# Kernel tuning notes

Hardware: AMD Instinct MI355X
Metric: run time of the kernel (lower is better)

The kernel has to match this reference:

```python
import jax, jax.numpy as jnp
import numpy as np


def setup_inputs() -> dict:
    key = jax.random.key(0)
    k1, k2, k3 = jax.random.split(key, 3)
    B, C, H, W = 32, 768, 24, 24
    feat1 = jax.random.normal(k1, (B, C, H, W), dtype=jnp.float32)
    feat2 = jax.random.normal(k2, (B, C, H, W), dtype=jnp.float32)
    gamma = jax.random.normal(k3, (1,), dtype=jnp.float32)
    return {"feat1": feat1, "feat2": feat2, "gamma": gamma}


def reference(feat1, feat2, gamma):
    # CMA: channel-wise cross-modal attention over flattened spatial dim.
    B, C, H, W = feat1.shape
    q = feat1.reshape(B, C, H * W)          # [B, C, HW]
    kv = feat2.reshape(B, C, H * W)         # [B, C, HW] (k and v share this)
    attn = jnp.einsum('bcn,bdn->bcd', q, kv)          # [B, C, C] = q @ k^T
    attn = jax.nn.softmax(attn, axis=-1)
    info = jnp.einsum('bcd,bdn->bcn', attn, kv)       # [B, C, HW]
    info = info.reshape(B, C, H, W)
    return gamma[0] * info + feat1
```

## Files before the change

kernel.cpp:

```cpp
#include <hip/hip_runtime.h>

#define B_  32
#define C_  768
#define HW_ 576

#define NCQ 18
#define NCP 24

typedef _Float16 half8 __attribute__((ext_vector_type(8)));
typedef _Float16 half4 __attribute__((ext_vector_type(4)));
typedef float    f32x4 __attribute__((ext_vector_type(4)));

__device__ __forceinline__ void g2l16(const void* g, void* l) {
    __builtin_amdgcn_global_load_lds(
        (const __attribute__((address_space(1))) unsigned int*)g,
        (__attribute__((address_space(3))) unsigned int*)l, 16, 0, 0);
}

#define VM(N) asm volatile("s_waitcnt vmcnt(" #N ")" ::: "memory")

__global__ __launch_bounds__(256) void prep_all(const float* __restrict__ f1,
                                                const float* __restrict__ f2,
                                                char* __restrict__ q16,
                                                char* __restrict__ kv16,
                                                char* __restrict__ vt,
                                                int b0, int cur, int nqk) {
    __shared__ float Vsh[32 * 201];
    const int bid = blockIdx.x;
    if (bid < nqk) {
        const int bz = bid % cur, u = bid / cur;
        int g   = u * 256 + threadIdx.x;
        int x   = g & 3;
        int row = (g >> 2) & 127;
        int t3  = g >> 9;
        int k0  = t3 % 18;
        int ti  = t3 / 18;
        int kc  = x ^ ((row >> 1) & 3);
        size_t src = ((size_t)(b0 + bz) * C_ + ti * 128 + row) * HW_ + k0 * 32 + kc * 8;
        f32x4 a0 = *(const f32x4*)(f1 + src);
        f32x4 a1 = *(const f32x4*)(f1 + src + 4);
        f32x4 c0 = *(const f32x4*)(f2 + src);
        f32x4 c1 = *(const f32x4*)(f2 + src + 4);
        half8 ha, hb;
        #pragma unroll
        for (int e = 0; e < 4; ++e) {
            ha[e] = (_Float16)a0[e]; ha[4 + e] = (_Float16)a1[e];
            hb[e] = (_Float16)c0[e]; hb[4 + e] = (_Float16)c1[e];
        }
        size_t dst = ((size_t)(((size_t)bz * 6 + ti) * 18 + k0) << 9) | (g & 511);
        *(half8*)(q16  + dst * 16) = ha;
        *(half8*)(kv16 + dst * 16) = hb;
    } else {
        int bid2 = bid - nqk;
        const int bz = bid2 % cur, u = bid2 / cur;
        int k0 = u / 3, tj = u % 3;
        int b  = b0 + bz;
        int t  = threadIdx.x;
        #pragma unroll
        for (int p = 0; p < 6; ++p) {
            int fidx = p * 256 + t;
            int dd = fidx / 48, c4 = fidx % 48;
            f32x4 v = *(const f32x4*)(f2 + ((size_t)b * C_ + k0 * 32 + dd) * HW_ + tj * 192 + c4 * 4);
            #pragma unroll
            for (int e = 0; e < 4; ++e) Vsh[dd * 201 + c4 * 4 + e] = v[e];
        }
        __syncthreads();
        char* ob = vt + ((size_t)(bz * 3 + tj) * NCP + k0) * 12288;
        #pragma unroll
        for (int p = 0; p < 3; ++p) {
            int o = p * 256 + t;
            int x = o & 3, n = o >> 2;
            int kc = x ^ ((n >> 1) & 3);
            half8 h;
            #pragma unroll
            for (int j = 0; j < 8; ++j) h[j] = (_Float16)Vsh[(kc * 8 + j) * 201 + n];
            *(half8*)(ob + o * 16) = h;
        }
    }
}

__global__ __launch_bounds__(512, 4) void qk6(const char* __restrict__ q16,
                                              const char* __restrict__ kv16,
                                              float* __restrict__ attn,
                                              float2* __restrict__ part,
                                              int cur) {
    __shared__ __align__(16) char S[3][24576];
    const int wg = blockIdx.x;
    const int bz = wg % cur, u = wg / cur;
    const int ti = u >> 2, tj = u & 3;
    const int t = threadIdx.x, lane = t & 63, w = t >> 6;
    const int rsub = lane >> 2, cb = (lane & 3) * 16;

    const char *p0, *p1, *p2;
    int o0, o1, o2;
    {
        auto arow = [&](int l) {
            int gr = ti * 192 + 16 * l + rsub;
            return q16 + ((size_t)(bz * 6 + (gr >> 7)) * NCQ) * 8192 + (gr & 127) * 64 + cb;
        };
        auto brow = [&](int l) {
            int gd = tj * 192 + 16 * l + rsub;
            return kv16 + ((size_t)(bz * 6 + (gd >> 7)) * NCQ) * 8192 + (gd & 127) * 64 + cb;
        };
        if (w < 4) {
            p0 = arow(2 * w);     o0 = (2 * w) * 1024;
            p1 = arow(2 * w + 1); o1 = (2 * w + 1) * 1024;
            p2 = brow(8 + w);     o2 = 12288 + (8 + w) * 1024;
        } else {
            int v = w - 4;
            p0 = brow(2 * v);     o0 = 12288 + (2 * v) * 1024;
            p1 = brow(2 * v + 1); o1 = 12288 + (2 * v + 1) * 1024;
            p2 = arow(8 + v);     o2 = (8 + v) * 1024;
        }
    }

    const int wr = (w >> 1) * 48, wc = (w & 1) * 96;
    const int r16 = lane & 15, cg = lane >> 4;
    int offA[3], offB[6];
    #pragma unroll
    for (int m = 0; m < 3; ++m) {
        int ra = wr + m * 16 + r16;
        offA[m] = ra * 64 + ((cg ^ ((ra >> 1) & 3)) << 4);
    }
    #pragma unroll
    for (int n = 0; n < 6; ++n) {
        int rb = wc + n * 16 + r16;
        offB[n] = 12288 + rb * 64 + ((cg ^ ((rb >> 1) & 3)) << 4);
    }

    f32x4 acc[3][6] = {};

#define STG(SLOT) do {                          \
        char* sb_ = &S[SLOT][0];                \
        g2l16(p0, sb_ + o0);                    \
        g2l16(p1, sb_ + o1);                    \
        g2l16(p2, sb_ + o2);                    \
        p0 += 8192; p1 += 8192; p2 += 8192;     \
    } while (0)

    STG(0); STG(1);
    int rd = 0, st = 2;
    for (int c = 0; c < NCQ; ++c) {
        if (c + 2 < NCQ) {
            STG(st); st = (st == 2) ? 0 : st + 1;
            VM(6);
        } else if (c + 2 == NCQ) {
            VM(3);
        } else {
            VM(0);
        }
        __builtin_amdgcn_s_barrier();
        const char* sb = &S[rd][0];
        rd = (rd == 2) ? 0 : rd + 1;
        half8 a0 = *(const half8*)(sb + offA[0]);
        half8 a1 = *(const half8*)(sb + offA[1]);
        half8 a2 = *(const half8*)(sb + offA[2]);
        __builtin_amdgcn_s_setprio(1);
        #pragma unroll
        for (int n = 0; n < 6; ++n) {
            half8 bn = *(const half8*)(sb + offB[n]);
            acc[0][n] = __builtin_amdgcn_mfma_f32_16x16x32_f16(a0, bn, acc[0][n], 0, 0, 0);
            acc[1][n] = __builtin_amdgcn_mfma_f32_16x16x32_f16(a1, bn, acc[1][n], 0, 0, 0);
            acc[2][n] = __builtin_amdgcn_mfma_f32_16x16x32_f16(a2, bn, acc[2][n], 0, 0, 0);
        }
        __builtin_amdgcn_s_setprio(0);
        __builtin_amdgcn_s_barrier();
    }
#undef STG

    float* ab = attn + ((size_t)bz * C_ + ti * 192) * C_ + tj * 192;
    const int col = lane & 15, rbase = (lane >> 4) * 4;
    #pragma unroll
    for (int m = 0; m < 3; ++m)
        #pragma unroll
        for (int n = 0; n < 6; ++n)
            #pragma unroll
            for (int rg = 0; rg < 4; ++rg)
                ab[(size_t)(wr + m * 16 + rbase + rg) * C_ + wc + n * 16 + col] = acc[m][n][rg];

    const int half = w & 1;
    #pragma unroll
    for (int m = 0; m < 3; ++m)
        #pragma unroll
        for (int rg = 0; rg < 4; ++rg) {
            float mx = -1e30f;
            #pragma unroll
            for (int n = 0; n < 6; ++n) mx = fmaxf(mx, acc[m][n][rg]);
            #pragma unroll
            for (int o = 1; o < 16; o <<= 1) mx = fmaxf(mx, __shfl_xor(mx, o));
            float s = 0.f;
            #pragma unroll
            for (int n = 0; n < 6; ++n) s += __expf(acc[m][n][rg] - mx);
            #pragma unroll
            for (int o = 1; o < 16; o <<= 1) s += __shfl_xor(s, o);
            if ((lane & 15) == 0) {
                int row = wr + m * 16 + (lane >> 4) * 4 + rg;
                part[((size_t)bz * C_ + ti * 192 + row) * 8 + tj * 2 + half] =
                    make_float2(mx, s);
            }
        }
}

__global__ __launch_bounds__(256) void sm_combine(const float2* __restrict__ part,
                                                  float2* __restrict__ stats,
                                                  const float* __restrict__ gamma,
                                                  int cur) {
    const int bid = blockIdx.x;
    const int bz = bid % cur, u = bid / cur;
    const int R = bz * C_ + u * 256 + threadIdx.x;
    float2 p[8];
    #pragma unroll
    for (int i = 0; i < 8; ++i) p[i] = part[(size_t)R * 8 + i];
    float m = p[0].x;
    #pragma unroll
    for (int i = 1; i < 8; ++i) m = fmaxf(m, p[i].x);
    float s = 0.f;
    #pragma unroll
    for (int i = 0; i < 8; ++i) s += p[i].y * __expf(p[i].x - m);
    stats[R] = make_float2(m, gamma[0] / s);
}

__global__ __launch_bounds__(512, 4) void pv10(const float* __restrict__ attn,
                                               const char* __restrict__ vt,
                                               const float2* __restrict__ stats,
                                               const float* __restrict__ f1,
                                               float* __restrict__ out,
                                               int b0, int cur) {
    __shared__ __align__(16) char S[4][20480];
    const int wg = blockIdx.x;
    const int bz = wg % cur, u = wg / cur;
    const int ti = u / 3, tj = u % 3;
    const int t = threadIdx.x, lane = t & 63, w = t >> 6;
    const int rsub = lane >> 2, cbb = (lane & 3) * 16;

    const int r0 = t >> 3;
    const int r1 = 64 + r0;
    const int d4 = t & 7;
    const float* srcA0 = attn + ((size_t)bz * C_ + ti * 128 + r0) * C_ + d4 * 4;
    const float* srcA1 = attn + ((size_t)bz * C_ + ti * 128 + r1) * C_ + d4 * 4;
    const float2 ms0 = stats[bz * C_ + ti * 128 + r0];
    const float2 ms1 = stats[bz * C_ + ti * 128 + r1];
    const int aw0 = r0 * 64 + (((d4 >> 1) ^ ((r0 >> 1) & 3)) << 4) + (d4 & 1) * 8;
    const int aw1 = r1 * 64 + (((d4 >> 1) ^ ((r1 >> 1) & 3)) << 4) + (d4 & 1) * 8;

    const char* vbase = vt + ((size_t)(bz * 3 + tj) * NCP) * 12288;
    const char *pB0, *pB1;
    int ob0, ob1;
    if (w < 4) {
        pB0 = vbase + (32 * w + rsub) * 64 + cbb;          ob0 = 8192 + (32 * w) * 64;
        pB1 = vbase + (32 * w + 16 + rsub) * 64 + cbb;     ob1 = 8192 + (32 * w + 16) * 64;
    } else {
        pB0 = vbase + (128 + 16 * (w - 4) + rsub) * 64 + cbb;
        ob0 = 8192 + (128 + 16 * (w - 4)) * 64;
        pB1 = vbase; ob1 = 0;
    }

    const int wr = (w >> 2) * 64, wc = (w & 3) * 48;
    const int r16 = lane & 15, cg = lane >> 4;
    int offA[4], offB[3];
    #pragma unroll
    for (int m = 0; m < 4; ++m) {
        int ra = wr + m * 16 + r16;
        offA[m] = ra * 64 + ((cg ^ ((ra >> 1) & 3)) << 4);
    }
    #pragma unroll
    for (int n = 0; n < 3; ++n) {
        int rb = wc + n * 16 + r16;
        offB[n] = 8192 + rb * 64 + ((cg ^ ((rb >> 1) & 3)) << 4);
    }

    f32x4 acc[4][3] = {};
    f32x4 vaA0, vaA1;
    f32x4 vaB0, vaB1;

#define STG_B(SLOT) do {                                  \
        g2l16(pB0, &S[SLOT][0] + ob0); pB0 += 12288;      \
        if (w < 4) { g2l16(pB1, &S[SLOT][0] + ob1); pB1 += 12288; } \
    } while (0)
#define LD_A(V0, V1) do { V0 = *(const f32x4*)srcA0; V1 = *(const f32x4*)srcA1; \
                          srcA0 += 32; srcA1 += 32; } while (0)
#define WR_A(SLOT, V0, V1) do {                                        \
        half4 h0, h1;                                                  \
        _Pragma("unroll")                                              \
        for (int e = 0; e < 4; ++e) {                                  \
            h0[e] = (_Float16)(__expf(V0[e] - ms0.x) * ms0.y);         \
            h1[e] = (_Float16)(__expf(V1[e] - ms1.x) * ms1.y);         \
        }                                                              \
        *(half4*)(&S[SLOT][0] + aw0) = h0;                             \
        *(half4*)(&S[SLOT][0] + aw1) = h1;                             \
    } while (0)
#define MFMA_SLOT(SB) do {                                             \
        const char* sb_ = (SB);                                        \
        half8 a_[4], b_[3];                                            \
        _Pragma("unroll")                                              \
        for (int m = 0; m < 4; ++m) a_[m] = *(const half8*)(sb_ + offA[m]); \
        _Pragma("unroll")                                              \
        for (int n = 0; n < 3; ++n) b_[n] = *(const half8*)(sb_ + offB[n]); \
        _Pragma("unroll")                                              \
        for (int m = 0; m < 4; ++m)                                    \
            _Pragma("unroll")                                          \
            for (int n = 0; n < 3; ++n)                                \
                acc[m][n] = __builtin_amdgcn_mfma_f32_16x16x32_f16(a_[m], b_[n], acc[m][n], 0, 0, 0); \
    } while (0)

    LD_A(vaA0, vaA1);
    WR_A(0, vaA0, vaA1);
    LD_A(vaB0, vaB1);
    WR_A(1, vaB0, vaB1);
    STG_B(0); STG_B(1);
    LD_A(vaA0, vaA1);
    LD_A(vaB0, vaB1);

    for (int p = 0; p < 12; ++p) {
        const int sa = (2 * p) & 3;
        asm volatile("s_waitcnt lgkmcnt(0)" ::: "memory");
        __builtin_amdgcn_s_barrier();
        if (p < 11) { STG_B((sa + 2) & 3); STG_B((sa + 3) & 3); }
        if (p < 11) { if (w < 4) VM(8); else VM(6); }
        else        { VM(0); }
        __builtin_amdgcn_s_barrier();

        __builtin_amdgcn_s_setprio(1);
        MFMA_SLOT(&S[sa][0]);
        MFMA_SLOT(&S[sa ^ 1][0]);
        __builtin_amdgcn_s_setprio(0);

        if (p < 11) {
            WR_A((sa + 2) & 3, vaA0, vaA1);
            WR_A((sa + 3) & 3, vaB0, vaB1);
            if (p < 10) {
                LD_A(vaA0, vaA1);
                LD_A(vaB0, vaB1);
            }
        }
    }
#undef MFMA_SLOT
#undef WR_A
#undef LD_A
#undef STG_B

    const int b = b0 + bz;
    const float* f1b = f1 + ((size_t)b * C_ + ti * 128) * HW_ + tj * 192;
    float*       ob  = out + ((size_t)b * C_ + ti * 128) * HW_ + tj * 192;
    const int col = lane & 15, rbase = (lane >> 4) * 4;
    #pragma unroll
    for (int m = 0; m < 4; ++m)
        #pragma unroll
        for (int n = 0; n < 3; ++n)
            #pragma unroll
            for (int rg = 0; rg < 4; ++rg) {
                int r2 = wr + m * 16 + rbase + rg;
                int c2 = wc + n * 16 + col;
                ob[(size_t)r2 * HW_ + c2] = acc[m][n][rg] + f1b[(size_t)r2 * HW_ + c2];
            }
}

extern "C" void kernel_launch(void* const* d_in, const int* in_sizes, int n_in,
                              void* d_out, int out_size, void* d_ws, size_t ws_size,
                              hipStream_t stream) {
    const float* feat1 = (const float*)d_in[0];
    const float* feat2 = (const float*)d_in[1];
    const float* gamma = (const float*)d_in[2];
    float* out = (float*)d_out;

    const size_t SZ_Q    = (size_t)C_ * HW_ * 2;
    const size_t SZ_ATTN = (size_t)C_ * C_  * 4;
    const size_t SZ_PART = (size_t)C_ * 8 * 8;
    const size_t SZ_ST   = (size_t)C_ * 8;
    const size_t per_batch = SZ_ATTN + 3 * SZ_Q + SZ_PART + SZ_ST;

    int nb = (int)(ws_size / per_batch);
    if (nb < 1) nb = 1;
    if (nb > B_) nb = B_;

    char* ws     = (char*)d_ws;
    float* attn  = (float*)ws;
    char* q16    = ws + (size_t)nb * SZ_ATTN;
    char* kv16   = q16 + (size_t)nb * SZ_Q;
    char* vtb    = kv16 + (size_t)nb * SZ_Q;
    float2* part = (float2*)(vtb + (size_t)nb * SZ_Q);
    float2* stats = (float2*)((char*)part + (size_t)nb * SZ_PART);

    for (int b0 = 0; b0 < B_; b0 += nb) {
        int cur = (B_ - b0 < nb) ? (B_ - b0) : nb;
        prep_all<<<cur * 288, 256, 0, stream>>>(feat1, feat2, q16, kv16, vtb, b0, cur, cur * 216);
        qk6<<<cur * 16, 512, 0, stream>>>(q16, kv16, attn, part, cur);
        sm_combine<<<cur * 3, 256, 0, stream>>>(part, stats, gamma, cur);
        pv10<<<cur * 18, 512, 0, stream>>>(attn, vtb, stats, feat1, out, b0, cur);
    }
}
```

Baseline: 141.2 us.

## Fuse Q fp32-to-fp16 conversion into the QK GEMM kernel

Removes the separate conversion of feat1 into a pre-swizzled fp16 workspace buffer. The QK kernel now loads fp32 Q rows straight from feat1 into registers, converts them to fp16 and writes them into the swizzled LDS stage, while K still arrives through async global-to-LDS loads. The software pipeline is restructured so register loads for Q are issued two stages ahead. This saves a full fp16 write and read of Q plus workspace, at the cost of more fp32 traffic per tile (each Q tile is re-read by several column blocks), more register pressure and extra synchronisation in the main loop.

New measurement: 177.0 us. 25.4% more time.

```diff
diff --git a/kernel.cpp b/kernel.cpp
--- a/kernel.cpp
+++ b/kernel.cpp
@@ -19,15 +19,13 @@
 
 #define VM(N) asm volatile("s_waitcnt vmcnt(" #N ")" ::: "memory")
 
-__global__ __launch_bounds__(256) void prep_all(const float* __restrict__ f1,
-                                                const float* __restrict__ f2,
-                                                char* __restrict__ q16,
-                                                char* __restrict__ kv16,
-                                                char* __restrict__ vt,
-                                                int b0, int cur, int nqk) {
+__global__ __launch_bounds__(256) void prep2(const float* __restrict__ f2,
+                                             char* __restrict__ kv16,
+                                             char* __restrict__ vt,
+                                             int b0, int cur, int nkv) {
     __shared__ float Vsh[32 * 201];
     const int bid = blockIdx.x;
-    if (bid < nqk) {
+    if (bid < nkv) {
         const int bz = bid % cur, u = bid / cur;
         int g   = u * 256 + threadIdx.x;
         int x   = g & 3;
@@ -37,21 +35,15 @@
         int ti  = t3 / 18;
         int kc  = x ^ ((row >> 1) & 3);
         size_t src = ((size_t)(b0 + bz) * C_ + ti * 128 + row) * HW_ + k0 * 32 + kc * 8;
-        f32x4 a0 = *(const f32x4*)(f1 + src);
-        f32x4 a1 = *(const f32x4*)(f1 + src + 4);
         f32x4 c0 = *(const f32x4*)(f2 + src);
         f32x4 c1 = *(const f32x4*)(f2 + src + 4);
-        half8 ha, hb;
-        #pragma unroll
-        for (int e = 0; e < 4; ++e) {
-            ha[e] = (_Float16)a0[e]; ha[4 + e] = (_Float16)a1[e];
-            hb[e] = (_Float16)c0[e]; hb[4 + e] = (_Float16)c1[e];
-        }
+        half8 hb;
+        #pragma unroll
+        for (int e = 0; e < 4; ++e) { hb[e] = (_Float16)c0[e]; hb[4 + e] = (_Float16)c1[e]; }
         size_t dst = ((size_t)(((size_t)bz * 6 + ti) * 18 + k0) << 9) | (g & 511);
-        *(half8*)(q16  + dst * 16) = ha;
         *(half8*)(kv16 + dst * 16) = hb;
     } else {
-        int bid2 = bid - nqk;
+        int bid2 = bid - nkv;
         const int bz = bid2 % cur, u = bid2 / cur;
         int k0 = u / 3, tj = u % 3;
         int b  = b0 + bz;
@@ -79,11 +71,11 @@
     }
 }
 
-__global__ __launch_bounds__(512, 4) void qk6(const char* __restrict__ q16,
-                                              const char* __restrict__ kv16,
-                                              float* __restrict__ attn,
-                                              float2* __restrict__ part,
-                                              int cur) {
+__global__ __launch_bounds__(512, 4) void qk14(const float* __restrict__ f1,
+                                               const char* __restrict__ kv16,
+                                               float* __restrict__ attn,
+                                               float2* __restrict__ part,
+                                               int b0, int cur) {
     __shared__ __align__(16) char S[3][24576];
     const int wg = blockIdx.x;
     const int bz = wg % cur, u = wg / cur;
@@ -91,28 +83,27 @@
     const int t = threadIdx.x, lane = t & 63, w = t >> 6;
     const int rsub = lane >> 2, cb = (lane & 3) * 16;
 
-    const char *p0, *p1, *p2;
-    int o0, o1, o2;
+    const char *pB0, *pB1 = nullptr;
+    int oB0, oB1 = 0;
     {
-        auto arow = [&](int l) {
-            int gr = ti * 192 + 16 * l + rsub;
-            return q16 + ((size_t)(bz * 6 + (gr >> 7)) * NCQ) * 8192 + (gr & 127) * 64 + cb;
-        };
         auto brow = [&](int l) {
             int gd = tj * 192 + 16 * l + rsub;
             return kv16 + ((size_t)(bz * 6 + (gd >> 7)) * NCQ) * 8192 + (gd & 127) * 64 + cb;
         };
         if (w < 4) {
-            p0 = arow(2 * w);     o0 = (2 * w) * 1024;
-            p1 = arow(2 * w + 1); o1 = (2 * w + 1) * 1024;
-            p2 = brow(8 + w);     o2 = 12288 + (8 + w) * 1024;
+            pB0 = brow(2 * w);     oB0 = 12288 + (2 * w) * 1024;
+            pB1 = brow(2 * w + 1); oB1 = 12288 + (2 * w + 1) * 1024;
         } else {
-            int v = w - 4;
-            p0 = brow(2 * v);     o0 = 12288 + (2 * v) * 1024;
-            p1 = brow(2 * v + 1); o1 = 12288 + (2 * v + 1) * 1024;
-            p2 = arow(8 + v);     o2 = (8 + v) * 1024;
+            pB0 = brow(8 + (w - 4)); oB0 = 12288 + (8 + (w - 4)) * 1024;
         }
     }
+
+    const int r0 = t >> 2, x0 = t & 3;
+    const int kc0 = x0 ^ ((r0 >> 1) & 3);
+    const float* srcA0 = f1 + ((size_t)(b0 + bz) * C_ + ti * 192 + r0) * HW_ + kc0 * 8;
+    const float* srcA1 = srcA0 + (size_t)128 * HW_;
+    const int aw0 = r0 * 64 + x0 * 16;
+    const int aw1 = aw0 + 8192;
 
     const int wr = (w >> 1) * 48, wc = (w & 1) * 96;
     const int r16 = lane & 15, cg = lane >> 4;
@@ -129,44 +120,77 @@
     }
 
     f32x4 acc[3][6] = {};
-
-#define STG(SLOT) do {                          \
-        char* sb_ = &S[SLOT][0];                \
-        g2l16(p0, sb_ + o0);                    \
-        g2l16(p1, sb_ + o1);                    \
-        g2l16(p2, sb_ + o2);                    \
-        p0 += 8192; p1 += 8192; p2 += 8192;     \
-    } while (0)
-
-    STG(0); STG(1);
-    int rd = 0, st = 2;
-    for (int c = 0; c < NCQ; ++c) {
-        if (c + 2 < NCQ) {
-            STG(st); st = (st == 2) ? 0 : st + 1;
-            VM(6);
-        } else if (c + 2 == NCQ) {
-            VM(3);
-        } else {
-            VM(0);
-        }
-        __builtin_amdgcn_s_barrier();
-        const char* sb = &S[rd][0];
-        rd = (rd == 2) ? 0 : rd + 1;
-        half8 a0 = *(const half8*)(sb + offA[0]);
-        half8 a1 = *(const half8*)(sb + offA[1]);
-        half8 a2 = *(const half8*)(sb + offA[2]);
-        __builtin_amdgcn_s_setprio(1);
-        #pragma unroll
-        for (int n = 0; n < 6; ++n) {
-            half8 bn = *(const half8*)(sb + offB[n]);
-            acc[0][n] = __builtin_amdgcn_mfma_f32_16x16x32_f16(a0, bn, acc[0][n], 0, 0, 0);
-            acc[1][n] = __builtin_amdgcn_mfma_f32_16x16x32_f16(a1, bn, acc[1][n], 0, 0, 0);
-            acc[2][n] = __builtin_amdgcn_mfma_f32_16x16x32_f16(a2, bn, acc[2][n], 0, 0, 0);
-        }
-        __builtin_amdgcn_s_setprio(0);
-        __builtin_amdgcn_s_barrier();
-    }
-#undef STG
+    f32x4 vaA0, vaA1, vaA2, vaA3;
+    f32x4 vaB0, vaB1, vaB2, vaB3;
+
+#define STG_B(SLOT) do {                                      \
+        g2l16(pB0, &S[SLOT][0] + oB0); pB0 += 8192;           \
+        if (w < 4) { g2l16(pB1, &S[SLOT][0] + oB1); pB1 += 8192; } \
+    } while (0)
+#define LD_A(V0, V1, V2, V3) do {                             \
+        V0 = *(const f32x4*)srcA0; V1 = *(const f32x4*)(srcA0 + 4); \
+        srcA0 += 32;                                          \
+        if (w < 4) { V2 = *(const f32x4*)srcA1;               \
+                     V3 = *(const f32x4*)(srcA1 + 4); srcA1 += 32; } \
+    } while (0)
+#define WR_A(SLOT, V0, V1, V2, V3) do {                       \
+        half8 h_;                                             \
+        _Pragma("unroll")                                     \
+        for (int e = 0; e < 4; ++e) { h_[e] = (_Float16)V0[e]; h_[4 + e] = (_Float16)V1[e]; } \
+        *(half8*)(&S[SLOT][0] + aw0) = h_;                    \
+        if (w < 4) {                                          \
+            half8 h2_;                                        \
+            _Pragma("unroll")                                 \
+            for (int e = 0; e < 4; ++e) { h2_[e] = (_Float16)V2[e]; h2_[4 + e] = (_Float16)V3[e]; } \
+            *(half8*)(&S[SLOT][0] + aw1) = h2_;               \
+        }                                                     \
+    } while (0)
+#define QMFMA(SLOT) do {                                      \
+        const char* sb_ = &S[SLOT][0];                        \
+        half8 a0 = *(const half8*)(sb_ + offA[0]);            \
+        half8 a1 = *(const half8*)(sb_ + offA[1]);            \
+        half8 a2 = *(const half8*)(sb_ + offA[2]);            \
+        __builtin_amdgcn_s_setprio(1);                        \
+        _Pragma("unroll")                                     \
+        for (int n = 0; n < 6; ++n) {                         \
+            half8 bn = *(const half8*)(sb_ + offB[n]);        \
+            acc[0][n] = __builtin_amdgcn_mfma_f32_16x16x32_f16(a0, bn, acc[0][n], 0, 0, 0); \
+            acc[1][n] = __builtin_amdgcn_mfma_f32_16x16x32_f16(a1, bn, acc[1][n], 0, 0, 0); \
+            acc[2][n] = __builtin_amdgcn_mfma_f32_16x16x32_f16(a2, bn, acc[2][n], 0, 0, 0); \
+        }                                                     \
+        __builtin_amdgcn_s_setprio(0);                        \
+    } while (0)
+#define QITER(W0,W1,W2,W3, L0,L1,L2,L3) do {                  \
+        asm volatile("s_waitcnt lgkmcnt(0)" ::: "memory");    \
+        __builtin_amdgcn_s_barrier();                         \
+        if (c + 2 < NCQ) STG_B((c + 2) % 3);                  \
+        if (c + 2 < NCQ)      { if (w < 4) VM(8); else VM(4); } \
+        else if (c + 1 < NCQ) { if (w < 4) VM(2); else VM(1); } \
+        else                  { VM(0); }                      \
+        __builtin_amdgcn_s_barrier();                         \
+        QMFMA(c % 3);                                         \
+        if (c + 2 < NCQ) WR_A((c + 2) % 3, W0, W1, W2, W3);   \
+        if (c + 3 < NCQ) LD_A(L0, L1, L2, L3);                \
+        ++c;                                                  \
+    } while (0)
+
+    LD_A(vaA0, vaA1, vaA2, vaA3);
+    WR_A(0, vaA0, vaA1, vaA2, vaA3);
+    LD_A(vaB0, vaB1, vaB2, vaB3);
+    WR_A(1, vaB0, vaB1, vaB2, vaB3);
+    STG_B(0); STG_B(1);
+    LD_A(vaA0, vaA1, vaA2, vaA3);
+
+    int c = 0;
+    for (int it = 0; it < 9; ++it) {
+        QITER(vaA0, vaA1, vaA2, vaA3, vaB0, vaB1, vaB2, vaB3);
+        QITER(vaB0, vaB1, vaB2, vaB3, vaA0, vaA1, vaA2, vaA3);
+    }
+#undef QITER
+#undef QMFMA
+#undef WR_A
+#undef LD_A
+#undef STG_B
 
     float* ab = attn + ((size_t)bz * C_ + ti * 192) * C_ + tj * 192;
     const int col = lane & 15, rbase = (lane >> 4) * 4;
@@ -363,11 +387,11 @@
     const float* gamma = (const float*)d_in[2];
     float* out = (float*)d_out;
 
-    const size_t SZ_Q    = (size_t)C_ * HW_ * 2;
+    const size_t SZ_KV   = (size_t)C_ * HW_ * 2;
     const size_t SZ_ATTN = (size_t)C_ * C_  * 4;
     const size_t SZ_PART = (size_t)C_ * 8 * 8;
     const size_t SZ_ST   = (size_t)C_ * 8;
-    const size_t per_batch = SZ_ATTN + 3 * SZ_Q + SZ_PART + SZ_ST;
+    const size_t per_batch = SZ_ATTN + 2 * SZ_KV + SZ_PART + SZ_ST;
 
     int nb = (int)(ws_size / per_batch);
     if (nb < 1) nb = 1;
@@ -375,16 +399,15 @@
 
     char* ws     = (char*)d_ws;
     float* attn  = (float*)ws;
-    char* q16    = ws + (size_t)nb * SZ_ATTN;
-    char* kv16   = q16 + (size_t)nb * SZ_Q;
-    char* vtb    = kv16 + (size_t)nb * SZ_Q;
-    float2* part = (float2*)(vtb + (size_t)nb * SZ_Q);
+    char* kv16   = ws + (size_t)nb * SZ_ATTN;
+    char* vtb    = kv16 + (size_t)nb * SZ_KV;
+    float2* part = (float2*)(vtb + (size_t)nb * SZ_KV);
     float2* stats = (float2*)((char*)part + (size_t)nb * SZ_PART);
 
     for (int b0 = 0; b0 < B_; b0 += nb) {
         int cur = (B_ - b0 < nb) ? (B_ - b0) : nb;
-        prep_all<<<cur * 288, 256, 0, stream>>>(feat1, feat2, q16, kv16, vtb, b0, cur, cur * 216);
-        qk6<<<cur * 16, 512, 0, stream>>>(q16, kv16, attn, part, cur);
+        prep2<<<cur * 288, 256, 0, stream>>>(feat2, kv16, vtb, b0, cur, cur * 216);
+        qk14<<<cur * 16, 512, 0, stream>>>(feat1, kv16, attn, part, b0, cur);
         sm_combine<<<cur * 3, 256, 0, stream>>>(part, stats, gamma, cur);
         pv10<<<cur * 18, 512, 0, stream>>>(attn, vtb, stats, feat1, out, b0, cur);
     }
```

## Store attention logits in tiled blocked layout for contiguous PV loads

Applied to the files above, without the earlier changes.

The QK kernel now writes fp32 logits into a blocked layout of 128x32 tiles, each contiguous, instead of row-major [C,C]. The PV kernel then reads each tile with one contiguous 32-byte chunk per thread and writes a single 16-byte fp16 vector to LDS, replacing two strided row loads and two 8-byte LDS stores. This aims to improve global load coalescing and cut LDS store instructions. In exchange the QK epilogue's stores become more scattered, and correctness depends on the stats/row mapping staying consistent with the new layout.

Result: no change. 142.7 us (+1.1%).

```diff
diff --git a/kernel.cpp b/kernel.cpp
--- a/kernel.cpp
+++ b/kernel.cpp
@@ -18,6 +18,7 @@
 }
 
 #define VM(N) asm volatile("s_waitcnt vmcnt(" #N ")" ::: "memory")
+
 
 __global__ __launch_bounds__(256) void prep_all(const float* __restrict__ f1,
                                                 const float* __restrict__ f2,
@@ -168,15 +169,18 @@
     }
 #undef STG
 
-    float* ab = attn + ((size_t)bz * C_ + ti * 192) * C_ + tj * 192;
     const int col = lane & 15, rbase = (lane >> 4) * 4;
     #pragma unroll
     for (int m = 0; m < 3; ++m)
         #pragma unroll
         for (int n = 0; n < 6; ++n)
             #pragma unroll
-            for (int rg = 0; rg < 4; ++rg)
-                ab[(size_t)(wr + m * 16 + rbase + rg) * C_ + wc + n * 16 + col] = acc[m][n][rg];
+            for (int rg = 0; rg < 4; ++rg) {
+                int grow = ti * 192 + wr + m * 16 + rbase + rg;
+                int gcol = tj * 192 + wc + n * 16 + col;
+                attn[(((size_t)bz * 6 + (grow >> 7)) * NCP + (gcol >> 5)) * 4096
+                     + (grow & 127) * 32 + (gcol & 31)] = acc[m][n][rg];
+            }
 
     const int half = w & 1;
     #pragma unroll
@@ -233,15 +237,11 @@
     const int t = threadIdx.x, lane = t & 63, w = t >> 6;
     const int rsub = lane >> 2, cbb = (lane & 3) * 16;
 
-    const int r0 = t >> 3;
-    const int r1 = 64 + r0;
-    const int d4 = t & 7;
-    const float* srcA0 = attn + ((size_t)bz * C_ + ti * 128 + r0) * C_ + d4 * 4;
-    const float* srcA1 = attn + ((size_t)bz * C_ + ti * 128 + r1) * C_ + d4 * 4;
+    const int r0 = t >> 2;
+    const int g4 = t & 3;
+    const float* srcA = attn + (((size_t)bz * 6 + ti) * NCP) * 4096 + t * 8;
     const float2 ms0 = stats[bz * C_ + ti * 128 + r0];
-    const float2 ms1 = stats[bz * C_ + ti * 128 + r1];
-    const int aw0 = r0 * 64 + (((d4 >> 1) ^ ((r0 >> 1) & 3)) << 4) + (d4 & 1) * 8;
-    const int aw1 = r1 * 64 + (((d4 >> 1) ^ ((r1 >> 1) & 3)) << 4) + (d4 & 1) * 8;
+    const int aw0 = r0 * 64 + ((g4 ^ ((r0 >> 1) & 3)) << 4);
 
     const char* vbase = vt + ((size_t)(bz * 3 + tj) * NCP) * 12288;
     const char *pB0, *pB1;
@@ -277,17 +277,16 @@
         g2l16(pB0, &S[SLOT][0] + ob0); pB0 += 12288;      \
         if (w < 4) { g2l16(pB1, &S[SLOT][0] + ob1); pB1 += 12288; } \
     } while (0)
-#define LD_A(V0, V1) do { V0 = *(const f32x4*)srcA0; V1 = *(const f32x4*)srcA1; \
-                          srcA0 += 32; srcA1 += 32; } while (0)
+#define LD_A(V0, V1) do { V0 = *(const f32x4*)srcA; V1 = *(const f32x4*)(srcA + 4); \
+                          srcA += 4096; } while (0)
 #define WR_A(SLOT, V0, V1) do {                                        \
-        half4 h0, h1;                                                  \
+        half8 h_;                                                      \
         _Pragma("unroll")                                              \
         for (int e = 0; e < 4; ++e) {                                  \
-            h0[e] = (_Float16)(__expf(V0[e] - ms0.x) * ms0.y);         \
-            h1[e] = (_Float16)(__expf(V1[e] - ms1.x) * ms1.y);         \
+            h_[e]     = (_Float16)(__expf(V0[e] - ms0.x) * ms0.y);     \
+            h_[4 + e] = (_Float16)(__expf(V1[e] - ms0.x) * ms0.y);     \
         }                                                              \
-        *(half4*)(&S[SLOT][0] + aw0) = h0;                             \
-        *(half4*)(&S[SLOT][0] + aw1) = h1;                             \
+        *(half8*)(&S[SLOT][0] + aw0) = h_;                             \
     } while (0)
 #define MFMA_SLOT(SB) do {                                             \
         const char* sb_ = (SB);                                        \
```
